# Optimization experiments

Measured on AMD Instinct MI355X. Metric: run time of the kernel, lower is better.

The kernel has to match this reference:

```python
import jax, jax.numpy as jnp
import numpy as np

NUM_HEADS = 16
EMBED_DIM = 1024
HEAD_DIM = EMBED_DIM // NUM_HEADS


def setup_inputs() -> dict:
    key = jax.random.key(0)
    ks = jax.random.split(key, 9)
    B, S, D = 2, 2048, EMBED_DIM
    s = 1.0 / np.sqrt(D)
    inp = {
        "x": jax.random.normal(ks[0], (B, S, D), dtype=jnp.float32),
        "Wq": jax.random.normal(ks[1], (D, D), dtype=jnp.float32) * s,
        "bq": jnp.zeros((D,), dtype=jnp.float32),
        "Wk": jax.random.normal(ks[2], (D, D), dtype=jnp.float32) * s,
        "bk": jnp.zeros((D,), dtype=jnp.float32),
        "Wv": jax.random.normal(ks[3], (D, D), dtype=jnp.float32) * s,
        "bv": jnp.zeros((D,), dtype=jnp.float32),
        "Wo": jax.random.normal(ks[4], (D, D), dtype=jnp.float32) * s,
        "bo": jnp.zeros((D,), dtype=jnp.float32),
    }
    return inp


def reference(x, Wq, bq, Wk, bk, Wv, bv, Wo, bo):
    B, S, D = x.shape
    H, Hd = NUM_HEADS, HEAD_DIM
    # projections (weights stored [in, out])
    q = (x @ Wq + bq).reshape(B, S, H, Hd).transpose(0, 2, 1, 3)  # [B,H,S,Hd]
    k = (x @ Wk + bk).reshape(B, S, H, Hd).transpose(0, 2, 1, 3)
    v = (x @ Wv + bv).reshape(B, S, H, Hd).transpose(0, 2, 1, 3)
    scores = jnp.einsum("bhqd,bhkd->bhqk", q, k) / jnp.sqrt(jnp.float32(Hd))
    causal = jnp.tril(jnp.ones((S, S), dtype=bool))  # True = keep
    scores = jnp.where(causal, scores, jnp.float32(-jnp.inf))
    attn = jax.nn.softmax(scores, axis=-1)
    ctx = jnp.einsum("bhqk,bhkd->bhqd", attn, v)  # [B,H,S,Hd]
    ctx = ctx.transpose(0, 2, 1, 3).reshape(B, S, D)
    return ctx @ Wo + bo
```

## Files before the change

kernel.cpp:

```cpp
#include <hip/hip_runtime.h>

#define NUMH 16
#define HD   64
#define SEQ  2048
#define NB   2
#define DIM  1024
#define MROWS (NB * SEQ)

typedef __attribute__((ext_vector_type(8))) short short8;
typedef __attribute__((ext_vector_type(4))) float f32x4;

__device__ inline unsigned short bf16_rn(float f) {
    unsigned u = __float_as_uint(f);
    return (unsigned short)((u + 0x7FFFu + ((u >> 16) & 1u)) >> 16);
}
__device__ inline float bf16f(unsigned short h) {
    return __uint_as_float(((unsigned)h) << 16);
}

__global__ void convert_split(const float* __restrict__ in,
                              unsigned short* __restrict__ hi,
                              unsigned short* __restrict__ lo, int n4)
{
    for (int i = blockIdx.x * blockDim.x + threadIdx.x; i < n4;
         i += gridDim.x * blockDim.x) {
        const float4 v = ((const float4*)in)[i];
        ushort4 h, l;
        h.x = bf16_rn(v.x); l.x = bf16_rn(v.x - bf16f(h.x));
        h.y = bf16_rn(v.y); l.y = bf16_rn(v.y - bf16f(h.y));
        h.z = bf16_rn(v.z); l.z = bf16_rn(v.z - bf16f(h.z));
        h.w = bf16_rn(v.w); l.w = bf16_rn(v.w - bf16f(h.w));
        ((ushort4*)hi)[i] = h;
        ((ushort4*)lo)[i] = l;
    }
}

__global__ __launch_bounds__(256)
void transpose_split(const float* __restrict__ W,
                     unsigned short* __restrict__ th,
                     unsigned short* __restrict__ tl)
{
    __shared__ float Ls[32][33];
    const int tx = threadIdx.x & 31, ty = threadIdx.x >> 5;
    const int k0 = blockIdx.x * 32, n0 = blockIdx.y * 32;
#pragma unroll
    for (int i = 0; i < 4; ++i)
        Ls[ty + 8 * i][tx] = W[(size_t)(k0 + ty + 8 * i) * DIM + n0 + tx];
    __syncthreads();
#pragma unroll
    for (int i = 0; i < 4; ++i) {
        const float f = Ls[tx][ty + 8 * i];
        const unsigned short h = bf16_rn(f);
        const unsigned short l = bf16_rn(f - bf16f(h));
        th[(size_t)(n0 + ty + 8 * i) * DIM + k0 + tx] = h;
        tl[(size_t)(n0 + ty + 8 * i) * DIM + k0 + tx] = l;
    }
}

template<int EPI>
__global__ __launch_bounds__(256, 2)
void gemm_split(const unsigned short* __restrict__ Ah,
                const unsigned short* __restrict__ Al,
                const unsigned short* __restrict__ Bh,
                const unsigned short* __restrict__ Bl,
                const float* __restrict__ bias,
                float* __restrict__ outF,
                unsigned short* __restrict__ outH,
                unsigned short* __restrict__ outL)
{
    __shared__ unsigned short AsH[128][32];
    __shared__ unsigned short AsL[128][32];
    __shared__ unsigned short BsH[64][32];
    __shared__ unsigned short BsL[64][32];

    const int tid  = threadIdx.x;
    const int m0   = blockIdx.x * 128;
    const int n0   = blockIdx.y * 64;
    const int wid  = tid >> 6;
    const int lane = tid & 63;
    const int wr   = wid >> 1;
    const int wc   = wid & 1;
    const int fr   = lane & 15;
    const int fg   = lane >> 4;
    const int K    = DIM;

    f32x4 acc[4][2];
#pragma unroll
    for (int i = 0; i < 4; ++i)
#pragma unroll
        for (int j = 0; j < 2; ++j) { f32x4 z = {0.f, 0.f, 0.f, 0.f}; acc[i][j] = z; }

    const int row0 = tid >> 2;
    const int k80  = (tid & 3) * 8;

    for (int kt = 0; kt < K; kt += 32) {
        __syncthreads();
        *(short8*)&AsH[row0][k80]      = *(const short8*)&Ah[(size_t)(m0 + row0) * K + kt + k80];
        *(short8*)&AsH[row0 + 64][k80] = *(const short8*)&Ah[(size_t)(m0 + row0 + 64) * K + kt + k80];
        *(short8*)&AsL[row0][k80]      = *(const short8*)&Al[(size_t)(m0 + row0) * K + kt + k80];
        *(short8*)&AsL[row0 + 64][k80] = *(const short8*)&Al[(size_t)(m0 + row0 + 64) * K + kt + k80];
        *(short8*)&BsH[row0][k80]      = *(const short8*)&Bh[(size_t)(n0 + row0) * K + kt + k80];
        *(short8*)&BsL[row0][k80]      = *(const short8*)&Bl[(size_t)(n0 + row0) * K + kt + k80];
        __syncthreads();

        short8 afh[4], afl[4], bfh[2], bfl[2];
#pragma unroll
        for (int i = 0; i < 4; ++i) {
            afh[i] = *(const short8*)&AsH[wr * 64 + i * 16 + fr][fg * 8];
            afl[i] = *(const short8*)&AsL[wr * 64 + i * 16 + fr][fg * 8];
        }
#pragma unroll
        for (int j = 0; j < 2; ++j) {
            bfh[j] = *(const short8*)&BsH[wc * 32 + j * 16 + fr][fg * 8];
            bfl[j] = *(const short8*)&BsL[wc * 32 + j * 16 + fr][fg * 8];
        }
#pragma unroll
        for (int i = 0; i < 4; ++i)
#pragma unroll
            for (int j = 0; j < 2; ++j) {
                acc[i][j] = __builtin_amdgcn_mfma_f32_16x16x32_bf16(afl[i], bfh[j], acc[i][j], 0, 0, 0);
                acc[i][j] = __builtin_amdgcn_mfma_f32_16x16x32_bf16(afh[i], bfl[j], acc[i][j], 0, 0, 0);
                acc[i][j] = __builtin_amdgcn_mfma_f32_16x16x32_bf16(afh[i], bfh[j], acc[i][j], 0, 0, 0);
            }
    }

#pragma unroll
    for (int i = 0; i < 4; ++i)
#pragma unroll
        for (int j = 0; j < 2; ++j) {
            const int col = n0 + wc * 32 + j * 16 + fr;
            const float bv = bias[col];
            if (EPI == 2) {
                const int row = m0 + wr * 64 + i * 16 + fg * 4;
                const int b  = row >> 11;
                const int s  = row & (SEQ - 1);
                const int hh = col >> 6;
                const int hd = col & (HD - 1);
                ushort4 pk;
                pk.x = bf16_rn(acc[i][j][0] + bv);
                pk.y = bf16_rn(acc[i][j][1] + bv);
                pk.z = bf16_rn(acc[i][j][2] + bv);
                pk.w = bf16_rn(acc[i][j][3] + bv);
                *(ushort4*)&outH[((size_t)(b * NUMH + hh) * HD + hd) * SEQ + s] = pk;
            } else {
#pragma unroll
                for (int r = 0; r < 4; ++r) {
                    const int row = m0 + wr * 64 + i * 16 + fg * 4 + r;
                    const float v = acc[i][j][r] + bv;
                    if (EPI == 0) {
                        outF[(size_t)row * DIM + col] = v;
                    } else {
                        const int b  = row >> 11;
                        const int s  = row & (SEQ - 1);
                        const int hh = col >> 6;
                        const int hd = col & (HD - 1);
                        const size_t idx = ((size_t)(b * NUMH + hh) * SEQ + s) * HD + hd;
                        const unsigned short hv = bf16_rn(v);
                        outH[idx] = hv;
                        outL[idx] = bf16_rn(v - bf16f(hv));
                    }
                }
            }
        }
}

__global__ __launch_bounds__(256, 3)
void attn_mfma(const unsigned short* __restrict__ Qh, const unsigned short* __restrict__ Ql,
               const unsigned short* __restrict__ Kh, const unsigned short* __restrict__ Kl,
               const unsigned short* __restrict__ Vt,
               unsigned short* __restrict__ ctxH, unsigned short* __restrict__ ctxL)
{
    __shared__ unsigned short KsH[64][72];
    __shared__ unsigned short KsL[64][72];
    __shared__ unsigned short Vs[64][72];
    __shared__ unsigned short Ps[4][16][72];

    const int tid  = threadIdx.x;
    const int w    = tid >> 6;
    const int lane = tid & 63;
    const int lc   = lane & 15;
    const int g    = lane >> 4;

    const int bh = blockIdx.x >> 5;
    const int qt = blockIdx.x & 31;
    const int q0 = qt * 64;
    const int bb = bh >> 4;
    const int hq = bh & 15;

    const size_t kqBase = (size_t)bh * SEQ * HD;
    const size_t vBase  = (size_t)bh * HD * SEQ;

    short8 qfh[2], qfl[2];
    {
        const size_t qr = kqBase + (size_t)(q0 + w * 16 + lc) * HD;
        qfh[0] = *(const short8*)&Qh[qr + g * 8];
        qfh[1] = *(const short8*)&Qh[qr + 32 + g * 8];
        qfl[0] = *(const short8*)&Ql[qr + g * 8];
        qfl[1] = *(const short8*)&Ql[qr + 32 + g * 8];
    }

    f32x4 o[4];
#pragma unroll
    for (int f4 = 0; f4 < 4; ++f4) { f32x4 z = {0.f, 0.f, 0.f, 0.f}; o[f4] = z; }
    float mrun[4], lrun[4];
#pragma unroll
    for (int r = 0; r < 4; ++r) { mrun[r] = -1e30f; lrun[r] = 0.f; }

    const int srow = w * 16 + (lane >> 2);
    const int scol = (lane & 3) * 16;

    for (int kt = 0; kt <= qt; ++kt) {
        const int k0 = kt * 64;
        __syncthreads();
        {
            const size_t kg = kqBase + (size_t)(k0 + srow) * HD + scol;
            const short8 a = *(const short8*)&Kh[kg];
            const short8 b = *(const short8*)&Kh[kg + 8];
            const short8 c = *(const short8*)&Kl[kg];
            const short8 d = *(const short8*)&Kl[kg + 8];
            const size_t vg = vBase + (size_t)srow * SEQ + k0 + scol;
            const short8 e = *(const short8*)&Vt[vg];
            const short8 f = *(const short8*)&Vt[vg + 8];
            *(short8*)&KsH[srow][scol]     = a;
            *(short8*)&KsH[srow][scol + 8] = b;
            *(short8*)&KsL[srow][scol]     = c;
            *(short8*)&KsL[srow][scol + 8] = d;
            *(short8*)&Vs[srow][scol]      = e;
            *(short8*)&Vs[srow][scol + 8]  = f;
        }
        __syncthreads();

        f32x4 sf[4];
#pragma unroll
        for (int f4 = 0; f4 < 4; ++f4) {
            f32x4 s = {0.f, 0.f, 0.f, 0.f};
#pragma unroll
            for (int s2 = 0; s2 < 2; ++s2) {
                const short8 kh = *(const short8*)&KsH[f4 * 16 + lc][s2 * 32 + g * 8];
                const short8 kl = *(const short8*)&KsL[f4 * 16 + lc][s2 * 32 + g * 8];
                s = __builtin_amdgcn_mfma_f32_16x16x32_bf16(qfl[s2], kh, s, 0, 0, 0);
                s = __builtin_amdgcn_mfma_f32_16x16x32_bf16(qfh[s2], kl, s, 0, 0, 0);
                s = __builtin_amdgcn_mfma_f32_16x16x32_bf16(qfh[s2], kh, s, 0, 0, 0);
            }
            sf[f4] = s;
        }

        const bool diag = (kt == qt);
        float rowm[4];
#pragma unroll
        for (int r = 0; r < 4; ++r) rowm[r] = -1e30f;
#pragma unroll
        for (int f4 = 0; f4 < 4; ++f4)
#pragma unroll
            for (int r = 0; r < 4; ++r) {
                float sv = sf[f4][r] * 0.125f;
                if (diag && (f4 * 16 + lc > w * 16 + g * 4 + r)) sv = -1e30f;
                sf[f4][r] = sv;
                rowm[r] = fmaxf(rowm[r], sv);
            }
#pragma unroll
        for (int off = 1; off < 16; off <<= 1)
#pragma unroll
            for (int r = 0; r < 4; ++r)
                rowm[r] = fmaxf(rowm[r], __shfl_xor(rowm[r], off));

        float psum[4];
#pragma unroll
        for (int r = 0; r < 4; ++r) {
            const float mn = fmaxf(mrun[r], rowm[r]);
            const float sc = __expf(mrun[r] - mn);
            mrun[r] = mn;
            lrun[r] *= sc;
            psum[r] = 0.f;
#pragma unroll
            for (int f4 = 0; f4 < 4; ++f4) o[f4][r] *= sc;
        }
#pragma unroll
        for (int f4 = 0; f4 < 4; ++f4)
#pragma unroll
            for (int r = 0; r < 4; ++r) {
                const float p = __expf(sf[f4][r] - mrun[r]);
                psum[r] += p;
                Ps[w][g * 4 + r][f4 * 16 + lc] = bf16_rn(p);
            }
#pragma unroll
        for (int off = 1; off < 16; off <<= 1)
#pragma unroll
            for (int r = 0; r < 4; ++r)
                psum[r] += __shfl_xor(psum[r], off);
#pragma unroll
        for (int r = 0; r < 4; ++r) lrun[r] += psum[r];

        asm volatile("s_waitcnt lgkmcnt(0)" ::: "memory");
        __builtin_amdgcn_sched_barrier(0);

        const short8 pa0 = *(const short8*)&Ps[w][lc][g * 8];
        const short8 pa1 = *(const short8*)&Ps[w][lc][32 + g * 8];
#pragma unroll
        for (int f4 = 0; f4 < 4; ++f4) {
            const short8 v0 = *(const short8*)&Vs[f4 * 16 + lc][g * 8];
            const short8 v1 = *(const short8*)&Vs[f4 * 16 + lc][32 + g * 8];
            o[f4] = __builtin_amdgcn_mfma_f32_16x16x32_bf16(pa0, v0, o[f4], 0, 0, 0);
            o[f4] = __builtin_amdgcn_mfma_f32_16x16x32_bf16(pa1, v1, o[f4], 0, 0, 0);
        }
    }

    float inv[4];
#pragma unroll
    for (int r = 0; r < 4; ++r) inv[r] = 1.f / lrun[r];
    const size_t orow0 = (size_t)bb * SEQ + q0 + w * 16 + g * 4;
#pragma unroll
    for (int r = 0; r < 4; ++r) {
        const size_t rbase = (orow0 + r) * DIM + hq * HD;
#pragma unroll
        for (int f4 = 0; f4 < 4; ++f4) {
            const float v = o[f4][r] * inv[r];
            const unsigned short hv = bf16_rn(v);
            ctxH[rbase + f4 * 16 + lc] = hv;
            ctxL[rbase + f4 * 16 + lc] = bf16_rn(v - bf16f(hv));
        }
    }
}

extern "C" void kernel_launch(void* const* d_in, const int* in_sizes, int n_in,
                              void* d_out, int out_size, void* d_ws, size_t ws_size,
                              hipStream_t stream)
{
    const float* x  = (const float*)d_in[0];
    const float* Wq = (const float*)d_in[1];
    const float* bq = (const float*)d_in[2];
    const float* Wk = (const float*)d_in[3];
    const float* bk = (const float*)d_in[4];
    const float* Wv = (const float*)d_in[5];
    const float* bv = (const float*)d_in[6];
    const float* Wo = (const float*)d_in[7];
    const float* bo = (const float*)d_in[8];

    char* base = (char*)d_ws;
    const size_t MB = 1024 * 1024;
    unsigned short* Qh_ = (unsigned short*)(base + 0 * MB);
    unsigned short* Ql_ = (unsigned short*)(base + 8 * MB);
    unsigned short* Kh_ = (unsigned short*)(base + 16 * MB);
    unsigned short* Kl_ = (unsigned short*)(base + 24 * MB);
    unsigned short* Vt_ = (unsigned short*)(base + 32 * MB);
    unsigned short* xh  = (unsigned short*)(base + 40 * MB);
    unsigned short* xl  = (unsigned short*)(base + 48 * MB);
    unsigned short* Wth = (unsigned short*)(base + 56 * MB);
    unsigned short* Wtl = (unsigned short*)(base + 58 * MB);

    dim3 blk(256);
    dim3 gg(MROWS / 128, DIM / 64);
    dim3 gt(DIM / 32, DIM / 32);

    hipLaunchKernelGGL(convert_split, dim3(2048), blk, 0, stream,
                       x, xh, xl, MROWS * DIM / 4);

    hipLaunchKernelGGL(transpose_split, gt, blk, 0, stream, Wq, Wth, Wtl);
    hipLaunchKernelGGL((gemm_split<1>), gg, blk, 0, stream,
                       xh, xl, Wth, Wtl, bq, nullptr, Qh_, Ql_);

    hipLaunchKernelGGL(transpose_split, gt, blk, 0, stream, Wk, Wth, Wtl);
    hipLaunchKernelGGL((gemm_split<1>), gg, blk, 0, stream,
                       xh, xl, Wth, Wtl, bk, nullptr, Kh_, Kl_);

    hipLaunchKernelGGL(transpose_split, gt, blk, 0, stream, Wv, Wth, Wtl);
    hipLaunchKernelGGL((gemm_split<2>), gg, blk, 0, stream,
                       xh, xl, Wth, Wtl, bv, nullptr, Vt_, nullptr);

    hipLaunchKernelGGL(attn_mfma, dim3(NB * NUMH * (SEQ / 64)), blk, 0, stream,
                       Qh_, Ql_, Kh_, Kl_, Vt_, xh, xl);

    hipLaunchKernelGGL(transpose_split, gt, blk, 0, stream, Wo, Wth, Wtl);
    hipLaunchKernelGGL((gemm_split<0>), gg, blk, 0, stream,
                       xh, xl, Wth, Wtl, bo, (float*)d_out, nullptr, nullptr);
}
```

Baseline: 375.0 us.

## Pair causal query tiles per block, swizzle LDS, prefetch tiles, fold softmax scale into Wq

The attention kernel now gives each block two query tiles (p and 31-p) so every block runs the same number of KV steps, and the K/V tiles it loads are shared by both. It uses transposed MFMA operands with an XOR-swizzled LDS layout, and moves P between lanes with ds_bpermute instead of a shared-memory round trip. Global loads for the next K/V tile are prefetched into registers in both the attention and GEMM kernels. The 1/sqrt(d) scale is folded into Wq and bq. These changes target causal load imbalance, LDS traffic and load latency, at the cost of higher register pressure (occupancy hint lowered from 3 to 2) and half as many attention blocks.

```diff
diff --git a/kernel.cpp b/kernel.cpp
--- a/kernel.cpp
+++ b/kernel.cpp
@@ -9,18 +9,19 @@
 
 typedef __attribute__((ext_vector_type(8))) short short8;
 typedef __attribute__((ext_vector_type(4))) float f32x4;
-
-__device__ inline unsigned short bf16_rn(float f) {
+typedef unsigned short u16;
+typedef unsigned int u32;
+
+__device__ inline u16 bf16_rn(float f) {
     unsigned u = __float_as_uint(f);
-    return (unsigned short)((u + 0x7FFFu + ((u >> 16) & 1u)) >> 16);
-}
-__device__ inline float bf16f(unsigned short h) {
+    return (u16)((u + 0x7FFFu + ((u >> 16) & 1u)) >> 16);
+}
+__device__ inline float bf16f(u16 h) {
     return __uint_as_float(((unsigned)h) << 16);
 }
 
 __global__ void convert_split(const float* __restrict__ in,
-                              unsigned short* __restrict__ hi,
-                              unsigned short* __restrict__ lo, int n4)
+                              u16* __restrict__ hi, u16* __restrict__ lo, int n4)
 {
     for (int i = blockIdx.x * blockDim.x + threadIdx.x; i < n4;
          i += gridDim.x * blockDim.x) {
@@ -37,8 +38,7 @@
 
 __global__ __launch_bounds__(256)
 void transpose_split(const float* __restrict__ W,
-                     unsigned short* __restrict__ th,
-                     unsigned short* __restrict__ tl)
+                     u16* __restrict__ th, u16* __restrict__ tl, float scale)
 {
     __shared__ float Ls[32][33];
     const int tx = threadIdx.x & 31, ty = threadIdx.x >> 5;
@@ -49,9 +49,9 @@
     __syncthreads();
 #pragma unroll
     for (int i = 0; i < 4; ++i) {
-        const float f = Ls[tx][ty + 8 * i];
-        const unsigned short h = bf16_rn(f);
-        const unsigned short l = bf16_rn(f - bf16f(h));
+        const float f = Ls[tx][ty + 8 * i] * scale;
+        const u16 h = bf16_rn(f);
+        const u16 l = bf16_rn(f - bf16f(h));
         th[(size_t)(n0 + ty + 8 * i) * DIM + k0 + tx] = h;
         tl[(size_t)(n0 + ty + 8 * i) * DIM + k0 + tx] = l;
     }
@@ -59,19 +59,16 @@
 
 template<int EPI>
 __global__ __launch_bounds__(256, 2)
-void gemm_split(const unsigned short* __restrict__ Ah,
-                const unsigned short* __restrict__ Al,
-                const unsigned short* __restrict__ Bh,
-                const unsigned short* __restrict__ Bl,
-                const float* __restrict__ bias,
-                float* __restrict__ outF,
-                unsigned short* __restrict__ outH,
-                unsigned short* __restrict__ outL)
+void gemm_split(const u16* __restrict__ Ah, const u16* __restrict__ Al,
+                const u16* __restrict__ Bh, const u16* __restrict__ Bl,
+                const float* __restrict__ bias, float bscale,
+                float* __restrict__ outF, u16* __restrict__ outH,
+                u16* __restrict__ outL)
 {
-    __shared__ unsigned short AsH[128][32];
-    __shared__ unsigned short AsL[128][32];
-    __shared__ unsigned short BsH[64][32];
-    __shared__ unsigned short BsL[64][32];
+    __shared__ u16 AsH[128][32];
+    __shared__ u16 AsL[128][32];
+    __shared__ u16 BsH[64][32];
+    __shared__ u16 BsL[64][32];
 
     const int tid  = threadIdx.x;
     const int m0   = blockIdx.x * 128;
@@ -93,15 +90,27 @@
     const int row0 = tid >> 2;
     const int k80  = (tid & 3) * 8;
 
+    short8 pf[6];
+    auto LOAD = [&](int kt) {
+        pf[0] = *(const short8*)&Ah[(size_t)(m0 + row0) * K + kt + k80];
+        pf[1] = *(const short8*)&Ah[(size_t)(m0 + row0 + 64) * K + kt + k80];
+        pf[2] = *(const short8*)&Al[(size_t)(m0 + row0) * K + kt + k80];
+        pf[3] = *(const short8*)&Al[(size_t)(m0 + row0 + 64) * K + kt + k80];
+        pf[4] = *(const short8*)&Bh[(size_t)(n0 + row0) * K + kt + k80];
+        pf[5] = *(const short8*)&Bl[(size_t)(n0 + row0) * K + kt + k80];
+    };
+    LOAD(0);
+
     for (int kt = 0; kt < K; kt += 32) {
         __syncthreads();
-        *(short8*)&AsH[row0][k80]      = *(const short8*)&Ah[(size_t)(m0 + row0) * K + kt + k80];
-        *(short8*)&AsH[row0 + 64][k80] = *(const short8*)&Ah[(size_t)(m0 + row0 + 64) * K + kt + k80];
-        *(short8*)&AsL[row0][k80]      = *(const short8*)&Al[(size_t)(m0 + row0) * K + kt + k80];
-        *(short8*)&AsL[row0 + 64][k80] = *(const short8*)&Al[(size_t)(m0 + row0 + 64) * K + kt + k80];
-        *(short8*)&BsH[row0][k80]      = *(const short8*)&Bh[(size_t)(n0 + row0) * K + kt + k80];
-        *(short8*)&BsL[row0][k80]      = *(const short8*)&Bl[(size_t)(n0 + row0) * K + kt + k80];
+        *(short8*)&AsH[row0][k80]      = pf[0];
+        *(short8*)&AsH[row0 + 64][k80] = pf[1];
+        *(short8*)&AsL[row0][k80]      = pf[2];
+        *(short8*)&AsL[row0 + 64][k80] = pf[3];
+        *(short8*)&BsH[row0][k80]      = pf[4];
+        *(short8*)&BsL[row0][k80]      = pf[5];
         __syncthreads();
+        if (kt + 32 < K) LOAD(kt + 32);
 
         short8 afh[4], afl[4], bfh[2], bfl[2];
 #pragma unroll
@@ -129,7 +138,7 @@
 #pragma unroll
         for (int j = 0; j < 2; ++j) {
             const int col = n0 + wc * 32 + j * 16 + fr;
-            const float bv = bias[col];
+            const float bv = bias[col] * bscale;
             if (EPI == 2) {
                 const int row = m0 + wr * 64 + i * 16 + fg * 4;
                 const int b  = row >> 11;
@@ -155,7 +164,7 @@
                         const int hh = col >> 6;
                         const int hd = col & (HD - 1);
                         const size_t idx = ((size_t)(b * NUMH + hh) * SEQ + s) * HD + hd;
-                        const unsigned short hv = bf16_rn(v);
+                        const u16 hv = bf16_rn(v);
                         outH[idx] = hv;
                         outL[idx] = bf16_rn(v - bf16f(hv));
                     }
@@ -164,16 +173,15 @@
         }
 }
 
-__global__ __launch_bounds__(256, 3)
-void attn_mfma(const unsigned short* __restrict__ Qh, const unsigned short* __restrict__ Ql,
-               const unsigned short* __restrict__ Kh, const unsigned short* __restrict__ Kl,
-               const unsigned short* __restrict__ Vt,
-               unsigned short* __restrict__ ctxH, unsigned short* __restrict__ ctxL)
+__global__ __launch_bounds__(256, 2)
+void attn_mfma2(const u16* __restrict__ Qh, const u16* __restrict__ Ql,
+                const u16* __restrict__ Kh, const u16* __restrict__ Kl,
+                const u16* __restrict__ Vt,
+                u16* __restrict__ ctxH, u16* __restrict__ ctxL)
 {
-    __shared__ unsigned short KsH[64][72];
-    __shared__ unsigned short KsL[64][72];
-    __shared__ unsigned short Vs[64][72];
-    __shared__ unsigned short Ps[4][16][72];
+    __shared__ u16 KsH[64 * 64];
+    __shared__ u16 KsL[64 * 64];
+    __shared__ u16 Vs [64 * 64];
 
     const int tid  = threadIdx.x;
     const int w    = tid >> 6;
@@ -181,144 +189,175 @@
     const int lc   = lane & 15;
     const int g    = lane >> 4;
 
-    const int bh = blockIdx.x >> 5;
-    const int qt = blockIdx.x & 31;
-    const int q0 = qt * 64;
-    const int bb = bh >> 4;
-    const int hq = bh & 15;
-
+    const int bh = blockIdx.x >> 4;
+    const int p  = blockIdx.x & 15;
+    const int qA = p, qB = 31 - p;
+    const int NT = 32 - p;
+    const int bb = bh >> 4, hq = bh & 15;
     const size_t kqBase = (size_t)bh * SEQ * HD;
     const size_t vBase  = (size_t)bh * HD * SEQ;
 
-    short8 qfh[2], qfl[2];
+    short8 qhA[2], qlA[2], qhB[2], qlB[2];
     {
-        const size_t qr = kqBase + (size_t)(q0 + w * 16 + lc) * HD;
-        qfh[0] = *(const short8*)&Qh[qr + g * 8];
-        qfh[1] = *(const short8*)&Qh[qr + 32 + g * 8];
-        qfl[0] = *(const short8*)&Ql[qr + g * 8];
-        qfl[1] = *(const short8*)&Ql[qr + 32 + g * 8];
-    }
-
-    f32x4 o[4];
-#pragma unroll
-    for (int f4 = 0; f4 < 4; ++f4) { f32x4 z = {0.f, 0.f, 0.f, 0.f}; o[f4] = z; }
-    float mrun[4], lrun[4];
-#pragma unroll
-    for (int r = 0; r < 4; ++r) { mrun[r] = -1e30f; lrun[r] = 0.f; }
-
-    const int srow = w * 16 + (lane >> 2);
-    const int scol = (lane & 3) * 16;
-
-    for (int kt = 0; kt <= qt; ++kt) {
-        const int k0 = kt * 64;
+        const size_t ra = kqBase + (size_t)(qA * 64 + w * 16 + lc) * HD;
+        const size_t rb = kqBase + (size_t)(qB * 64 + w * 16 + lc) * HD;
+        qhA[0] = *(const short8*)&Qh[ra + g * 8];  qhA[1] = *(const short8*)&Qh[ra + 32 + g * 8];
+        qlA[0] = *(const short8*)&Ql[ra + g * 8];  qlA[1] = *(const short8*)&Ql[ra + 32 + g * 8];
+        qhB[0] = *(const short8*)&Qh[rb + g * 8];  qhB[1] = *(const short8*)&Qh[rb + 32 + g * 8];
+        qlB[0] = *(const short8*)&Ql[rb + g * 8];  qlB[1] = *(const short8*)&Ql[rb + 32 + g * 8];
+    }
+
+    f32x4 oA[4], oB[4];
+#pragma unroll
+    for (int f4 = 0; f4 < 4; ++f4) {
+        f32x4 z = {0.f, 0.f, 0.f, 0.f};
+        oA[f4] = z; oB[f4] = z;
+    }
+    float mA = -1e30f, lA = 0.f, mB = -1e30f, lB = 0.f;
+
+    const int srow = tid >> 2;
+    const int scol = (tid & 3) * 16;
+    const int sw   = (srow & 7) << 3;
+    const int so1  = srow * 64 + (scol ^ sw);
+    const int so2  = srow * 64 + ((scol + 8) ^ sw);
+    const int rsw  = (lc & 7) << 3;
+
+    short8 pf[6];
+    auto LOADT = [&](int kt) {
+        const size_t kg = kqBase + (size_t)(kt * 64 + srow) * HD + scol;
+        pf[0] = *(const short8*)&Kh[kg];      pf[1] = *(const short8*)&Kh[kg + 8];
+        pf[2] = *(const short8*)&Kl[kg];      pf[3] = *(const short8*)&Kl[kg + 8];
+        const size_t vg = vBase + (size_t)srow * SEQ + kt * 64 + scol;
+        pf[4] = *(const short8*)&Vt[vg];      pf[5] = *(const short8*)&Vt[vg + 8];
+    };
+    LOADT(0);
+
+    for (int kt = 0; kt < NT; ++kt) {
         __syncthreads();
-        {
-            const size_t kg = kqBase + (size_t)(k0 + srow) * HD + scol;
-            const short8 a = *(const short8*)&Kh[kg];
-            const short8 b = *(const short8*)&Kh[kg + 8];
-            const short8 c = *(const short8*)&Kl[kg];
-            const short8 d = *(const short8*)&Kl[kg + 8];
-            const size_t vg = vBase + (size_t)srow * SEQ + k0 + scol;
-            const short8 e = *(const short8*)&Vt[vg];
-            const short8 f = *(const short8*)&Vt[vg + 8];
-            *(short8*)&KsH[srow][scol]     = a;
-            *(short8*)&KsH[srow][scol + 8] = b;
-            *(short8*)&KsL[srow][scol]     = c;
-            *(short8*)&KsL[srow][scol + 8] = d;
-            *(short8*)&Vs[srow][scol]      = e;
-            *(short8*)&Vs[srow][scol + 8]  = f;
-        }
+        *(short8*)&KsH[so1] = pf[0];  *(short8*)&KsH[so2] = pf[1];
+        *(short8*)&KsL[so1] = pf[2];  *(short8*)&KsL[so2] = pf[3];
+        *(short8*)&Vs [so1] = pf[4];  *(short8*)&Vs [so2] = pf[5];
         __syncthreads();
-
-        f32x4 sf[4];
+        if (kt + 1 < NT) LOADT(kt + 1);
+
+        const bool actA = (kt <= qA);
+        const int  k0   = kt * 64;
+
+        f32x4 sA[4], sB[4];
 #pragma unroll
         for (int f4 = 0; f4 < 4; ++f4) {
-            f32x4 s = {0.f, 0.f, 0.f, 0.f};
+            f32x4 a = {0.f, 0.f, 0.f, 0.f}, b = {0.f, 0.f, 0.f, 0.f};
 #pragma unroll
             for (int s2 = 0; s2 < 2; ++s2) {
-                const short8 kh = *(const short8*)&KsH[f4 * 16 + lc][s2 * 32 + g * 8];
-                const short8 kl = *(const short8*)&KsL[f4 * 16 + lc][s2 * 32 + g * 8];
-                s = __builtin_amdgcn_mfma_f32_16x16x32_bf16(qfl[s2], kh, s, 0, 0, 0);
-                s = __builtin_amdgcn_mfma_f32_16x16x32_bf16(qfh[s2], kl, s, 0, 0, 0);
-                s = __builtin_amdgcn_mfma_f32_16x16x32_bf16(qfh[s2], kh, s, 0, 0, 0);
+                const int off = (f4 * 16 + lc) * 64 + ((s2 * 32 + g * 8) ^ rsw);
+                const short8 kh = *(const short8*)&KsH[off];
+                const short8 kl = *(const short8*)&KsL[off];
+                if (actA) {
+                    a = __builtin_amdgcn_mfma_f32_16x16x32_bf16(kh, qlA[s2], a, 0, 0, 0);
+                    a = __builtin_amdgcn_mfma_f32_16x16x32_bf16(kl, qhA[s2], a, 0, 0, 0);
+                    a = __builtin_amdgcn_mfma_f32_16x16x32_bf16(kh, qhA[s2], a, 0, 0, 0);
+                }
+                b = __builtin_amdgcn_mfma_f32_16x16x32_bf16(kh, qlB[s2], b, 0, 0, 0);
+                b = __builtin_amdgcn_mfma_f32_16x16x32_bf16(kl, qhB[s2], b, 0, 0, 0);
+                b = __builtin_amdgcn_mfma_f32_16x16x32_bf16(kh, qhB[s2], b, 0, 0, 0);
             }
-            sf[f4] = s;
-        }
-
-        const bool diag = (kt == qt);
-        float rowm[4];
-#pragma unroll
-        for (int r = 0; r < 4; ++r) rowm[r] = -1e30f;
-#pragma unroll
-        for (int f4 = 0; f4 < 4; ++f4)
-#pragma unroll
-            for (int r = 0; r < 4; ++r) {
-                float sv = sf[f4][r] * 0.125f;
-                if (diag && (f4 * 16 + lc > w * 16 + g * 4 + r)) sv = -1e30f;
-                sf[f4][r] = sv;
-                rowm[r] = fmaxf(rowm[r], sv);
+            sA[f4] = a; sB[f4] = b;
+        }
+
+        u32 pbA[2][4], pbB[2][4];
+        const int a0 = (((g & 1) * 2 + 0) * 16 + lc) * 4;
+        const int a1 = (((g & 1) * 2 + 1) * 16 + lc) * 4;
+        const bool hi = ((g >> 1) & 1) != 0;
+
+        auto SOFTMAX = [&](f32x4* sf, float& m, float& l, f32x4* o,
+                           int qt, u32 pb[2][4]) {
+            const bool diag = (kt == qt);
+            const int  qg   = qt * 64 + w * 16 + lc;
+            float pm = -1e30f;
+#pragma unroll
+            for (int f4 = 0; f4 < 4; ++f4)
+#pragma unroll
+                for (int r = 0; r < 4; ++r) {
+                    float sv = sf[f4][r];
+                    if (diag && (k0 + f4 * 16 + g * 4 + r > qg)) sv = -1e30f;
+                    sf[f4][r] = sv;
+                    pm = fmaxf(pm, sv);
+                }
+            pm = fmaxf(pm, __shfl_xor(pm, 16));
+            pm = fmaxf(pm, __shfl_xor(pm, 32));
+            const float mn = fmaxf(m, pm);
+            const float sc = __expf(m - mn);
+            m = mn; l *= sc;
+#pragma unroll
+            for (int f4 = 0; f4 < 4; ++f4) o[f4] *= sc;
+            float ps = 0.f;
+            u32 pk[4][2];
+#pragma unroll
+            for (int f4 = 0; f4 < 4; ++f4)
+#pragma unroll
+                for (int pr = 0; pr < 2; ++pr) {
+                    const float p0 = __expf(sf[f4][pr * 2 + 0] - mn);
+                    const float p1 = __expf(sf[f4][pr * 2 + 1] - mn);
+                    ps += p0 + p1;
+                    pk[f4][pr] = (u32)bf16_rn(p0) | ((u32)bf16_rn(p1) << 16);
+                }
+            ps += __shfl_xor(ps, 16);
+            ps += __shfl_xor(ps, 32);
+            l += ps;
+#pragma unroll
+            for (int s2 = 0; s2 < 2; ++s2)
+#pragma unroll
+                for (int mm = 0; mm < 4; ++mm) {
+                    const int addr = (mm < 2) ? a0 : a1;
+                    const u32 t0 = (u32)__builtin_amdgcn_ds_bpermute(addr, (int)pk[s2 * 2 + 0][mm & 1]);
+                    const u32 t1 = (u32)__builtin_amdgcn_ds_bpermute(addr, (int)pk[s2 * 2 + 1][mm & 1]);
+                    pb[s2][mm] = hi ? t1 : t0;
+                }
+        };
+
+        if (actA) SOFTMAX(sA, mA, lA, oA, qA, pbA);
+        SOFTMAX(sB, mB, lB, oB, qB, pbB);
+
+#pragma unroll
+        for (int s2 = 0; s2 < 2; ++s2) {
+            union { u32 u[4]; short8 s; } ua, ub;
+#pragma unroll
+            for (int mm = 0; mm < 4; ++mm) { ua.u[mm] = pbA[s2][mm]; ub.u[mm] = pbB[s2][mm]; }
+#pragma unroll
+            for (int f4 = 0; f4 < 4; ++f4) {
+                const int off = (f4 * 16 + lc) * 64 + ((s2 * 32 + g * 8) ^ rsw);
+                const short8 vv = *(const short8*)&Vs[off];
+                if (actA) oA[f4] = __builtin_amdgcn_mfma_f32_16x16x32_bf16(vv, ua.s, oA[f4], 0, 0, 0);
+                oB[f4] = __builtin_amdgcn_mfma_f32_16x16x32_bf16(vv, ub.s, oB[f4], 0, 0, 0);
             }
-#pragma unroll
-        for (int off = 1; off < 16; off <<= 1)
-#pragma unroll
-            for (int r = 0; r < 4; ++r)
-                rowm[r] = fmaxf(rowm[r], __shfl_xor(rowm[r], off));
-
-        float psum[4];
+        }
+    }
+
+    const float iA = 1.f / lA, iB = 1.f / lB;
+    const size_t rowA = (size_t)bb * SEQ + qA * 64 + w * 16 + lc;
+    const size_t rowB = (size_t)bb * SEQ + qB * 64 + w * 16 + lc;
+#pragma unroll
+    for (int f4 = 0; f4 < 4; ++f4) {
+        const int colb = hq * HD + f4 * 16 + g * 4;
+        ushort4 h4, l4;
 #pragma unroll
         for (int r = 0; r < 4; ++r) {
-            const float mn = fmaxf(mrun[r], rowm[r]);
-            const float sc = __expf(mrun[r] - mn);
-            mrun[r] = mn;
-            lrun[r] *= sc;
-            psum[r] = 0.f;
-#pragma unroll
-            for (int f4 = 0; f4 < 4; ++f4) o[f4][r] *= sc;
-        }
-#pragma unroll
-        for (int f4 = 0; f4 < 4; ++f4)
-#pragma unroll
-            for (int r = 0; r < 4; ++r) {
-                const float p = __expf(sf[f4][r] - mrun[r]);
-                psum[r] += p;
-                Ps[w][g * 4 + r][f4 * 16 + lc] = bf16_rn(p);
-            }
-#pragma unroll
-        for (int off = 1; off < 16; off <<= 1)
-#pragma unroll
-            for (int r = 0; r < 4; ++r)
-                psum[r] += __shfl_xor(psum[r], off);
-#pragma unroll
-        for (int r = 0; r < 4; ++r) lrun[r] += psum[r];
-
-        asm volatile("s_waitcnt lgkmcnt(0)" ::: "memory");
-        __builtin_amdgcn_sched_barrier(0);
-
-        const short8 pa0 = *(const short8*)&Ps[w][lc][g * 8];
-        const short8 pa1 = *(const short8*)&Ps[w][lc][32 + g * 8];
-#pragma unroll
-        for (int f4 = 0; f4 < 4; ++f4) {
-            const short8 v0 = *(const short8*)&Vs[f4 * 16 + lc][g * 8];
-            const short8 v1 = *(const short8*)&Vs[f4 * 16 + lc][32 + g * 8];
-            o[f4] = __builtin_amdgcn_mfma_f32_16x16x32_bf16(pa0, v0, o[f4], 0, 0, 0);
-            o[f4] = __builtin_amdgcn_mfma_f32_16x16x32_bf16(pa1, v1, o[f4], 0, 0, 0);
-        }
-    }
-
-    float inv[4];
-#pragma unroll
-    for (int r = 0; r < 4; ++r) inv[r] = 1.f / lrun[r];
-    const size_t orow0 = (size_t)bb * SEQ + q0 + w * 16 + g * 4;
-#pragma unroll
-    for (int r = 0; r < 4; ++r) {
-        const size_t rbase = (orow0 + r) * DIM + hq * HD;
-#pragma unroll
-        for (int f4 = 0; f4 < 4; ++f4) {
-            const float v = o[f4][r] * inv[r];
-            const unsigned short hv = bf16_rn(v);
-            ctxH[rbase + f4 * 16 + lc] = hv;
-            ctxL[rbase + f4 * 16 + lc] = bf16_rn(v - bf16f(hv));
-        }
+            const float v = oA[f4][r] * iA;
+            const u16 hv = bf16_rn(v);
+            ((u16*)&h4)[r] = hv;
+            ((u16*)&l4)[r] = bf16_rn(v - bf16f(hv));
+        }
+        *(ushort4*)&ctxH[rowA * DIM + colb] = h4;
+        *(ushort4*)&ctxL[rowA * DIM + colb] = l4;
+#pragma unroll
+        for (int r = 0; r < 4; ++r) {
+            const float v = oB[f4][r] * iB;
+            const u16 hv = bf16_rn(v);
+            ((u16*)&h4)[r] = hv;
+            ((u16*)&l4)[r] = bf16_rn(v - bf16f(hv));
+        }
+        *(ushort4*)&ctxH[rowB * DIM + colb] = h4;
+        *(ushort4*)&ctxL[rowB * DIM + colb] = l4;
     }
 }
 
@@ -338,15 +377,15 @@
 
     char* base = (char*)d_ws;
     const size_t MB = 1024 * 1024;
-    unsigned short* Qh_ = (unsigned short*)(base + 0 * MB);
-    unsigned short* Ql_ = (unsigned short*)(base + 8 * MB);
-    unsigned short* Kh_ = (unsigned short*)(base + 16 * MB);
-    unsigned short* Kl_ = (unsigned short*)(base + 24 * MB);
-    unsigned short* Vt_ = (unsigned short*)(base + 32 * MB);
-    unsigned short* xh  = (unsigned short*)(base + 40 * MB);
-    unsigned short* xl  = (unsigned short*)(base + 48 * MB);
-    unsigned short* Wth = (unsigned short*)(base + 56 * MB);
-    unsigned short* Wtl = (unsigned short*)(base + 58 * MB);
+    u16* Qh_ = (u16*)(base + 0 * MB);
+    u16* Ql_ = (u16*)(base + 8 * MB);
+    u16* Kh_ = (u16*)(base + 16 * MB);
+    u16* Kl_ = (u16*)(base + 24 * MB);
+    u16* Vt_ = (u16*)(base + 32 * MB);
+    u16* xh  = (u16*)(base + 40 * MB);
+    u16* xl  = (u16*)(base + 48 * MB);
+    u16* Wth = (u16*)(base + 56 * MB);
+    u16* Wtl = (u16*)(base + 58 * MB);
 
     dim3 blk(256);
     dim3 gg(MROWS / 128, DIM / 64);
@@ -355,22 +394,22 @@
     hipLaunchKernelGGL(convert_split, dim3(2048), blk, 0, stream,
                        x, xh, xl, MROWS * DIM / 4);
 
-    hipLaunchKernelGGL(transpose_split, gt, blk, 0, stream, Wq, Wth, Wtl);
+    hipLaunchKernelGGL(transpose_split, gt, blk, 0, stream, Wq, Wth, Wtl, 0.125f);
     hipLaunchKernelGGL((gemm_split<1>), gg, blk, 0, stream,
-                       xh, xl, Wth, Wtl, bq, nullptr, Qh_, Ql_);
-
-    hipLaunchKernelGGL(transpose_split, gt, blk, 0, stream, Wk, Wth, Wtl);
+                       xh, xl, Wth, Wtl, bq, 0.125f, nullptr, Qh_, Ql_);
+
+    hipLaunchKernelGGL(transpose_split, gt, blk, 0, stream, Wk, Wth, Wtl, 1.0f);
     hipLaunchKernelGGL((gemm_split<1>), gg, blk, 0, stream,
-                       xh, xl, Wth, Wtl, bk, nullptr, Kh_, Kl_);
-
-    hipLaunchKernelGGL(transpose_split, gt, blk, 0, stream, Wv, Wth, Wtl);
+                       xh, xl, Wth, Wtl, bk, 1.0f, nullptr, Kh_, Kl_);
+
+    hipLaunchKernelGGL(transpose_split, gt, blk, 0, stream, Wv, Wth, Wtl, 1.0f);
     hipLaunchKernelGGL((gemm_split<2>), gg, blk, 0, stream,
-                       xh, xl, Wth, Wtl, bv, nullptr, Vt_, nullptr);
-
-    hipLaunchKernelGGL(attn_mfma, dim3(NB * NUMH * (SEQ / 64)), blk, 0, stream,
+                       xh, xl, Wth, Wtl, bv, 1.0f, nullptr, Vt_, nullptr);
+
+    hipLaunchKernelGGL(attn_mfma2, dim3(NB * NUMH * 16), blk, 0, stream,
                        Qh_, Ql_, Kh_, Kl_, Vt_, xh, xl);
 
-    hipLaunchKernelGGL(transpose_split, gt, blk, 0, stream, Wo, Wth, Wtl);
+    hipLaunchKernelGGL(transpose_split, gt, blk, 0, stream, Wo, Wth, Wtl, 1.0f);
     hipLaunchKernelGGL((gemm_split<0>), gg, blk, 0, stream,
-                       xh, xl, Wth, Wtl, bo, (float*)d_out, nullptr, nullptr);
-}
+                       xh, xl, Wth, Wtl, bo, 1.0f, (float*)d_out, nullptr, nullptr);
+}
```

After: 324.4 us. 13.5% less time.
